# Optimization experiments

Hardware: AMD Instinct MI355X
Metric: run time of the kernel (lower is better)

Reference implementation:

```python
import jax, jax.numpy as jnp
import numpy as np

NUM_EMBEDDINGS = 8192
EMBEDDING_DIM = 256


def setup_inputs() -> dict:
    key = jax.random.key(0)
    k1, k2 = jax.random.split(key)
    z = jax.random.normal(k1, (8, 4096, EMBEDDING_DIM), dtype=jnp.float32)
    # codebook initialized uniform(-1/K, 1/K) as in the torch module
    embeddings = jax.random.uniform(
        k2, (NUM_EMBEDDINGS, EMBEDDING_DIM), dtype=jnp.float32,
        minval=-1.0 / NUM_EMBEDDINGS, maxval=1.0 / NUM_EMBEDDINGS)
    return {"z": z, "embeddings": embeddings}


def reference(z, embeddings):
    # flat_z: [N, D]
    flat_z = z.reshape(-1, EMBEDDING_DIM)
    # squared L2 distances: ||z||^2 - 2 z E^T + ||E||^2  -> [N, K]
    distances = (
        jnp.sum(flat_z ** 2, axis=1, keepdims=True)
        - 2.0 * jnp.einsum('nd,kd->nk', flat_z, embeddings)
        + jnp.sum(embeddings ** 2, axis=1)
    )
    encoding_indices = jnp.argmin(distances, axis=1)  # [N]
    quantized = embeddings[encoding_indices].reshape(z.shape)
    return quantized
```

## Files before the change

### kernel.cpp

```cpp
#include <hip/hip_runtime.h>


#define KCODES 8192
#define DIM    256
#define NROWS  32768
#define BM     128
#define KT     256
#define CAPL   64
#define CAPG   16

typedef __attribute__((ext_vector_type(8))) short short8_t;
typedef __attribute__((ext_vector_type(4))) float f32x4_t;

__device__ __forceinline__ unsigned cvt_pk_bf16(float lo, float hi)
{
    unsigned r;
    asm("v_cvt_pk_bf16_f32 %0, %1, %2" : "=v"(r) : "v"(lo), "v"(hi));
    return r;
}

__device__ __forceinline__ unsigned fmap(float f)
{
    unsigned u = __float_as_uint(f);
    return (u & 0x80000000u) ? ~u : (u | 0x80000000u);
}
__device__ __forceinline__ float funmap(unsigned m)
{
    unsigned u = (m & 0x80000000u) ? (m & 0x7fffffffu) : ~m;
    return __uint_as_float(u);
}

__device__ __forceinline__ float np_sumsq_256(const float* __restrict__ x)
{
    float blk[2];
#pragma unroll
    for (int b = 0; b < 2; ++b) {
        const float* p = x + 128 * b;
        float r[8];
        float4 v0 = *reinterpret_cast<const float4*>(p);
        float4 v1 = *reinterpret_cast<const float4*>(p + 4);
        r[0] = __fmul_rn(v0.x, v0.x); r[1] = __fmul_rn(v0.y, v0.y);
        r[2] = __fmul_rn(v0.z, v0.z); r[3] = __fmul_rn(v0.w, v0.w);
        r[4] = __fmul_rn(v1.x, v1.x); r[5] = __fmul_rn(v1.y, v1.y);
        r[6] = __fmul_rn(v1.z, v1.z); r[7] = __fmul_rn(v1.w, v1.w);
        for (int i = 8; i < 128; i += 8) {
            float4 w0 = *reinterpret_cast<const float4*>(p + i);
            float4 w1 = *reinterpret_cast<const float4*>(p + i + 4);
            r[0] = __fadd_rn(r[0], __fmul_rn(w0.x, w0.x));
            r[1] = __fadd_rn(r[1], __fmul_rn(w0.y, w0.y));
            r[2] = __fadd_rn(r[2], __fmul_rn(w0.z, w0.z));
            r[3] = __fadd_rn(r[3], __fmul_rn(w0.w, w0.w));
            r[4] = __fadd_rn(r[4], __fmul_rn(w1.x, w1.x));
            r[5] = __fadd_rn(r[5], __fmul_rn(w1.y, w1.y));
            r[6] = __fadd_rn(r[6], __fmul_rn(w1.z, w1.z));
            r[7] = __fadd_rn(r[7], __fmul_rn(w1.w, w1.w));
        }
        blk[b] = __fadd_rn(__fadd_rn(__fadd_rn(r[0], r[1]), __fadd_rn(r[2], r[3])),
                           __fadd_rn(__fadd_rn(r[4], r[5]), __fadd_rn(r[6], r[7])));
    }
    return __fadd_rn(blk[0], blk[1]);
}

__global__ void vq_rowsq(const float* __restrict__ X, float* __restrict__ out, int nrows)
{
    const int r = blockIdx.x * blockDim.x + threadIdx.x;
    if (r < nrows) out[r] = np_sumsq_256(X + (size_t)r * DIM);
}

__global__ __launch_bounds__(512, 2)
void vq_p1(const float* __restrict__ z, const float* __restrict__ E,
           const float* __restrict__ A32, const float* __restrict__ C32,
           int* __restrict__ counts, unsigned short* __restrict__ candg,
           int* __restrict__ badcnt, int* __restrict__ badlist)
{
    __shared__ unsigned short zsh[BM * 256];
    __shared__ unsigned short esh[KT * 64];
    __shared__ float cbuf[KT];
    __shared__ float scandT[BM * CAPL];
    __shared__ unsigned short scandK[BM * CAPL];
    __shared__ int scnt[BM];
    __shared__ unsigned rminu[BM];

    const int tid  = threadIdx.x;
    const int lane = tid & 63;
    const int wave = tid >> 6;
    const int wr = wave >> 2;
    const int wc = wave & 3;
    const int l15 = lane & 15, l4 = lane >> 4;
    const int rowBase = blockIdx.x * BM;

    {
        const int r = tid >> 2, hf = tid & 3;
        const float* zp = z + (size_t)(rowBase + r) * DIM + hf * 64;
#pragma unroll
        for (int i = 0; i < 16; ++i) {
            float4 v = reinterpret_cast<const float4*>(zp)[i];
            unsigned lo = cvt_pk_bf16(v.x, v.y), hi = cvt_pk_bf16(v.z, v.w);
            const int slot = hf * 8 + (i >> 1);
            const int sub  = (i & 1) * 4;
            *reinterpret_cast<uint2*>(&zsh[r * 256 + ((slot ^ (r & 7)) << 3) + sub]) =
                make_uint2(lo, hi);
        }
    }
    if (tid < BM) { scnt[tid] = 0; rminu[tid] = 0xFFFFFFFFu; }

    float runm[16], Wv[16];
#pragma unroll
    for (int rf = 0; rf < 4; ++rf)
#pragma unroll
        for (int reg = 0; reg < 4; ++reg) {
            const float a = A32[rowBase + 64 * wr + 16 * rf + 4 * l4 + reg];
            const unsigned ebits = (__float_as_uint(a) >> 23) & 255u;
            Wv[rf * 4 + reg] = __uint_as_float((ebits - 19u) << 23);
            runm[rf * 4 + reg] = 1e30f;
        }
    __syncthreads();

#pragma unroll 1
    for (int kt = 0; kt < KCODES; kt += KT) {
        f32x4_t acc[4][4];
#pragma unroll
        for (int rf = 0; rf < 4; ++rf)
#pragma unroll
            for (int cf = 0; cf < 4; ++cf) acc[rf][cf] = (f32x4_t){0.f, 0.f, 0.f, 0.f};

#pragma unroll 1
        for (int c = 0; c < 4; ++c) {
            __syncthreads();
            if (c == 0 && tid < KT) cbuf[tid] = C32[kt + tid];
#pragma unroll
            for (int i = 0; i < 8; ++i) {
                const int gi = i * 512 + tid;
                const int code = gi >> 4, dp = gi & 15;
                float4 v = *reinterpret_cast<const float4*>(
                    &E[(size_t)(kt + code) * DIM + c * 64 + dp * 4]);
                unsigned lo = cvt_pk_bf16(v.x, v.y), hi = cvt_pk_bf16(v.z, v.w);
                const int slot = dp >> 1, sub = (dp & 1) * 4;
                *reinterpret_cast<uint2*>(
                    &esh[code * 64 + ((slot ^ (code & 7)) << 3) + sub]) = make_uint2(lo, hi);
            }
            __syncthreads();
#pragma unroll
            for (int ks = 0; ks < 2; ++ks) {
                short8_t a[4], b[4];
#pragma unroll
                for (int rf = 0; rf < 4; ++rf) {
                    const int row = 64 * wr + 16 * rf + l15;
                    const int slot = 8 * c + 4 * ks + l4;
                    a[rf] = *reinterpret_cast<const short8_t*>(
                        &zsh[row * 256 + ((slot ^ (row & 7)) << 3)]);
                }
#pragma unroll
                for (int cf = 0; cf < 4; ++cf) {
                    const int code = 64 * wc + 16 * cf + l15;
                    const int slot = 4 * ks + l4;
                    b[cf] = *reinterpret_cast<const short8_t*>(
                        &esh[code * 64 + ((slot ^ (code & 7)) << 3)]);
                }
#pragma unroll
                for (int rf = 0; rf < 4; ++rf)
#pragma unroll
                    for (int cf = 0; cf < 4; ++cf)
                        acc[rf][cf] = __builtin_amdgcn_mfma_f32_16x16x32_bf16(
                            a[rf], b[cf], acc[rf][cf], 0, 0, 0);
            }
        }

#pragma unroll
        for (int rf = 0; rf < 4; ++rf) {
#pragma unroll
            for (int reg = 0; reg < 4; ++reg) {
                float t[4];
#pragma unroll
                for (int cf = 0; cf < 4; ++cf)
                    t[cf] = fmaf(-2.0f, acc[rf][cf][reg], cbuf[64 * wc + 16 * cf + l15]);
                float m = fminf(fminf(t[0], t[1]), fminf(t[2], t[3]));
                m = fminf(m, __shfl_xor(m, 1));
                m = fminf(m, __shfl_xor(m, 2));
                m = fminf(m, __shfl_xor(m, 4));
                m = fminf(m, __shfl_xor(m, 8));
                const int idx = rf * 4 + reg;
                const int rl = 64 * wr + 16 * rf + 4 * l4 + reg;
                float rm = fminf(runm[idx], m);
                if (l15 == 0) atomicMin(&rminu[rl], fmap(rm));
                rm = fminf(rm, funmap(rminu[rl]));
                runm[idx] = rm;
                const float thr = rm + Wv[idx];
#pragma unroll
                for (int cf = 0; cf < 4; ++cf) {
                    if (t[cf] <= thr) {
                        const int ai = atomicAdd(&scnt[rl], 1);
                        if (ai < CAPL) {
                            scandT[rl * CAPL + ai] = t[cf];
                            scandK[rl * CAPL + ai] =
                                (unsigned short)(kt + 64 * wc + 16 * cf + l15);
                        }
                    }
                }
            }
        }
    }

    __syncthreads();
    if (tid < BM) {
        const int row = rowBase + tid;
        const float a = A32[row];
        const unsigned ebits = (__float_as_uint(a) >> 23) & 255u;
        const float Wr = __uint_as_float((ebits - 19u) << 23);
        const float thrF = funmap(rminu[tid]) + Wr;
        const int n = scnt[tid];
        bool bad = (n > CAPL);
        int m = 0;
        if (!bad) {
            for (int i = 0; i < n; ++i) {
                if (scandT[tid * CAPL + i] <= thrF) {
                    if (m < CAPG) candg[(size_t)row * CAPG + m] = scandK[tid * CAPL + i];
                    ++m;
                }
            }
            bad = (m > CAPG);
        }
        counts[row] = bad ? -1 : m;
        if (bad) badlist[atomicAdd(badcnt, 1)] = row;
    }
}

__global__ __launch_bounds__(256)
void vq_p2(const float* __restrict__ z, const float* __restrict__ E,
           const float* __restrict__ A32, const float* __restrict__ C32,
           const int* __restrict__ counts, const unsigned short* __restrict__ candg,
           int* __restrict__ widx)
{
    __shared__ float zsh[4][256];
    const int lane = threadIdx.x & 63;
    const int w = threadIdx.x >> 6;
    const int row = blockIdx.x * 4 + w;
    const int cnt = counts[row];
    if (cnt == 1) {
        if (lane == 0) widx[row] = (int)candg[(size_t)row * CAPG];
        return;
    }
    if (cnt <= 0 || cnt > CAPG) return;
    {
        float4 v = *reinterpret_cast<const float4*>(&z[(size_t)row * DIM + lane * 4]);
        *reinterpret_cast<float4*>(&zsh[w][lane * 4]) = v;
    }
    asm volatile("s_waitcnt lgkmcnt(0)" ::: "memory");
    __builtin_amdgcn_sched_barrier(0);
    const int cl = lane < cnt ? lane : cnt - 1;
    const int myk = (int)candg[(size_t)row * CAPG + cl];
    const float* er = E + (size_t)myk * DIM;
    float s0 = 0.f, s1 = 0.f, s2 = 0.f, s3 = 0.f;
#pragma unroll 16
    for (int t = 0; t < 64; ++t) {
        const float4 ev = *reinterpret_cast<const float4*>(er + 4 * t);
        const float4 zv = *reinterpret_cast<const float4*>(&zsh[w][4 * t]);
        s0 = __fadd_rn(s0, __fmul_rn(zv.x, ev.x));
        s1 = __fadd_rn(s1, __fmul_rn(zv.y, ev.y));
        s2 = __fadd_rn(s2, __fmul_rn(zv.z, ev.z));
        s3 = __fadd_rn(s3, __fmul_rn(zv.w, ev.w));
    }
    const float dot = __fadd_rn(__fadd_rn(s0, s1), __fadd_rn(s2, s3));
    const float dist = __fadd_rn(__fsub_rn(A32[row], 2.0f * dot), C32[myk]);
    unsigned long long key =
        ((unsigned long long)__float_as_uint(dist) << 13) | (unsigned)myk;
    if (lane >= cnt) key = ~0ull;
#pragma unroll
    for (int off = 1; off < 64; off <<= 1) {
        const unsigned long long ok = __shfl_xor(key, off);
        key = ok < key ? ok : key;
    }
    if (lane == 0) widx[row] = (int)(key & (KCODES - 1));
}

__global__ __launch_bounds__(1024)
void vq_pfull(const float* __restrict__ z, const float* __restrict__ E,
              const float* __restrict__ A32, const float* __restrict__ C32,
              const int* __restrict__ badcnt, const int* __restrict__ badlist,
              int* __restrict__ widx)
{
    __shared__ float zsh[256];
    __shared__ unsigned long long skey;
    const int tid = threadIdx.x;
    const int nbad = *badcnt;
    for (int it = blockIdx.x; it < nbad; it += gridDim.x) {
        const int row = badlist[it];
        if (tid == 0) skey = ~0ull;
        if (tid < 64) {
            float4 v = *reinterpret_cast<const float4*>(&z[(size_t)row * DIM + tid * 4]);
            *reinterpret_cast<float4*>(&zsh[tid * 4]) = v;
        }
        __syncthreads();
        const float Ar = A32[row];
        unsigned long long best = ~0ull;
#pragma unroll 1
        for (int i = 0; i < KCODES / 1024; ++i) {
            const int k = i * 1024 + tid;
            const float* er = E + (size_t)k * DIM;
            float s0 = 0.f, s1 = 0.f, s2 = 0.f, s3 = 0.f;
#pragma unroll 16
            for (int t = 0; t < 64; ++t) {
                const float4 ev = *reinterpret_cast<const float4*>(er + 4 * t);
                const float4 zv = *reinterpret_cast<const float4*>(&zsh[4 * t]);
                s0 = __fadd_rn(s0, __fmul_rn(zv.x, ev.x));
                s1 = __fadd_rn(s1, __fmul_rn(zv.y, ev.y));
                s2 = __fadd_rn(s2, __fmul_rn(zv.z, ev.z));
                s3 = __fadd_rn(s3, __fmul_rn(zv.w, ev.w));
            }
            const float dot = __fadd_rn(__fadd_rn(s0, s1), __fadd_rn(s2, s3));
            const float dist = __fadd_rn(__fsub_rn(Ar, 2.0f * dot), C32[k]);
            const unsigned long long key =
                ((unsigned long long)__float_as_uint(dist) << 13) | (unsigned)k;
            best = key < best ? key : best;
        }
#pragma unroll
        for (int off = 1; off < 64; off <<= 1) {
            const unsigned long long ok = __shfl_xor(best, off);
            best = ok < best ? ok : best;
        }
        if ((tid & 63) == 0) atomicMin(&skey, best);
        __syncthreads();
        if (tid == 0) widx[row] = (int)(skey & (KCODES - 1));
        __syncthreads();
    }
}

__global__ void vq_gather(const float* __restrict__ E, const int* __restrict__ widx,
                          float* __restrict__ out)
{
    const int gid = blockIdx.x * 256 + threadIdx.x;
    const int n  = gid >> 6;
    const int d4 = gid & 63;
    const int k = widx[n] & (KCODES - 1);
    reinterpret_cast<float4*>(out)[(size_t)n * 64 + d4] =
        reinterpret_cast<const float4*>(E)[(size_t)k * 64 + d4];
}

extern "C" void kernel_launch(void* const* d_in, const int* in_sizes, int n_in,
                              void* d_out, int out_size, void* d_ws, size_t ws_size,
                              hipStream_t stream)
{
    const float* zp = (const float*)d_in[0];
    const float* Ep = (const float*)d_in[1];
    float* out = (float*)d_out;
    char* ws = (char*)d_ws;

    float* A32    = (float*)ws;
    float* C32    = (float*)(ws + 131072);
    int*   widx   = (int*)(ws + 163840);
    int*   counts = (int*)(ws + 294912);
    int*   badcnt = (int*)(ws + 425984);
    int*   badlist = (int*)(ws + 426000);
    unsigned short* candg = (unsigned short*)(ws + 557072);

    hipMemsetAsync(badcnt, 0, 4, stream);
    vq_rowsq<<<NROWS / 256, 256, 0, stream>>>(zp, A32, NROWS);
    vq_rowsq<<<KCODES / 256, 256, 0, stream>>>(Ep, C32, KCODES);
    vq_p1<<<NROWS / BM, 512, 0, stream>>>(zp, Ep, A32, C32, counts, candg, badcnt, badlist);
    vq_p2<<<NROWS / 4, 256, 0, stream>>>(zp, Ep, A32, C32, counts, candg, widx);
    vq_pfull<<<512, 1024, 0, stream>>>(zp, Ep, A32, C32, badcnt, badlist, widx);
    vq_gather<<<NROWS * (DIM / 4) / 256, 256, 0, stream>>>(Ep, widx, out);
}
```

Before: 528.2 us.

## Pre-convert codebook to swizzled bf16 and double-buffer it via async LDS loads

Adds a kernel that converts the codebook to bf16 once, already laid out in the swizzled tile order that the main kernel expects, and stores it in the output buffer as scratch. The distance kernel now double-buffers codebook chunks in LDS using global_load_lds direct-to-LDS copies, which overlaps loading with MFMA work and cuts the synchronisations per chunk from two to one. Per-block conversion work is removed. The candidate list also drops the stored distance values and the final re-filtering pass, keeping up to 32 candidate indices directly. This can send more rows to the slower fallback path and relies on the output buffer being free until the gather kernel overwrites it.

New measurement: 664.3 us. +25.8%, slower.

```diff
diff --git a/kernel.cpp b/kernel.cpp
--- a/kernel.cpp
+++ b/kernel.cpp
@@ -6,8 +6,8 @@
 #define NROWS  32768
 #define BM     128
 #define KT     256
-#define CAPL   64
-#define CAPG   16
+#define NSTEP  128
+#define CAPG   32
 
 typedef __attribute__((ext_vector_type(8))) short short8_t;
 typedef __attribute__((ext_vector_type(4))) float f32x4_t;
@@ -17,6 +17,13 @@
     unsigned r;
     asm("v_cvt_pk_bf16_f32 %0, %1, %2" : "=v"(r) : "v"(lo), "v"(hi));
     return r;
+}
+
+__device__ __forceinline__ void gload_lds16(const void* g, void* l)
+{
+    __builtin_amdgcn_global_load_lds(
+        (const __attribute__((address_space(1))) unsigned int*)g,
+        (__attribute__((address_space(3))) unsigned int*)l, 16, 0, 0);
 }
 
 __device__ __forceinline__ unsigned fmap(float f)
@@ -67,17 +74,34 @@
     if (r < nrows) out[r] = np_sumsq_256(X + (size_t)r * DIM);
 }
 
+__global__ void vq_cvtE(const float* __restrict__ E, unsigned short* __restrict__ Ebf)
+{
+    const int gid = blockIdx.x * 256 + threadIdx.x;
+    const int code_g = gid >> 5;
+    const int sg = gid & 31;
+    const int c = sg >> 3, slot = sg & 7;
+    const int ktIdx = code_g >> 8, code = code_g & 255;
+    const float* src = E + (size_t)code_g * DIM + c * 64 + slot * 8;
+    const float4 v0 = *reinterpret_cast<const float4*>(src);
+    const float4 v1 = *reinterpret_cast<const float4*>(src + 4);
+    uint4 w;
+    w.x = cvt_pk_bf16(v0.x, v0.y); w.y = cvt_pk_bf16(v0.z, v0.w);
+    w.z = cvt_pk_bf16(v1.x, v1.y); w.w = cvt_pk_bf16(v1.z, v1.w);
+    unsigned short* dst = Ebf + (size_t)(ktIdx * 4 + c) * 16384
+                        + code * 64 + ((slot ^ (code & 7)) << 3);
+    *reinterpret_cast<uint4*>(dst) = w;
+}
+
 __global__ __launch_bounds__(512, 2)
-void vq_p1(const float* __restrict__ z, const float* __restrict__ E,
+void vq_p1(const float* __restrict__ z, const unsigned short* __restrict__ Ebf,
            const float* __restrict__ A32, const float* __restrict__ C32,
            int* __restrict__ counts, unsigned short* __restrict__ candg,
            int* __restrict__ badcnt, int* __restrict__ badlist)
 {
     __shared__ unsigned short zsh[BM * 256];
-    __shared__ unsigned short esh[KT * 64];
+    __shared__ unsigned short esh[2][KT * 64];
     __shared__ float cbuf[KT];
-    __shared__ float scandT[BM * CAPL];
-    __shared__ unsigned short scandK[BM * CAPL];
+    __shared__ unsigned short scandK[BM * CAPG];
     __shared__ int scnt[BM];
     __shared__ unsigned rminu[BM];
 
@@ -114,114 +138,107 @@
             Wv[rf * 4 + reg] = __uint_as_float((ebits - 19u) << 23);
             runm[rf * 4 + reg] = 1e30f;
         }
+
+    {
+        const char* g = reinterpret_cast<const char*>(Ebf) + tid * 16;
+        char* l = reinterpret_cast<char*>(&esh[0][0]) + wave * 1024;
+#pragma unroll
+        for (int i = 0; i < 4; ++i)
+            gload_lds16(g + i * 8192, l + i * 8192);
+    }
     __syncthreads();
 
+    f32x4_t acc[4][4];
 #pragma unroll 1
-    for (int kt = 0; kt < KCODES; kt += KT) {
-        f32x4_t acc[4][4];
-#pragma unroll
-        for (int rf = 0; rf < 4; ++rf)
-#pragma unroll
-            for (int cf = 0; cf < 4; ++cf) acc[rf][cf] = (f32x4_t){0.f, 0.f, 0.f, 0.f};
-
-#pragma unroll 1
-        for (int c = 0; c < 4; ++c) {
-            __syncthreads();
-            if (c == 0 && tid < KT) cbuf[tid] = C32[kt + tid];
-#pragma unroll
-            for (int i = 0; i < 8; ++i) {
-                const int gi = i * 512 + tid;
-                const int code = gi >> 4, dp = gi & 15;
-                float4 v = *reinterpret_cast<const float4*>(
-                    &E[(size_t)(kt + code) * DIM + c * 64 + dp * 4]);
-                unsigned lo = cvt_pk_bf16(v.x, v.y), hi = cvt_pk_bf16(v.z, v.w);
-                const int slot = dp >> 1, sub = (dp & 1) * 4;
-                *reinterpret_cast<uint2*>(
-                    &esh[code * 64 + ((slot ^ (code & 7)) << 3) + sub]) = make_uint2(lo, hi);
+    for (int s = 0; s < NSTEP; ++s) {
+        const int cur = s & 1;
+        const int c = s & 3;
+        if (c == 0) {
+#pragma unroll
+            for (int rf = 0; rf < 4; ++rf)
+#pragma unroll
+                for (int cf = 0; cf < 4; ++cf) acc[rf][cf] = (f32x4_t){0.f, 0.f, 0.f, 0.f};
+            if (tid < KT) cbuf[tid] = C32[(s >> 2) * KT + tid];
+        }
+        if (s + 1 < NSTEP) {
+            const char* g = reinterpret_cast<const char*>(Ebf)
+                          + (size_t)(s + 1) * 32768 + tid * 16;
+            char* l = reinterpret_cast<char*>(&esh[cur ^ 1][0]) + wave * 1024;
+#pragma unroll
+            for (int i = 0; i < 4; ++i)
+                gload_lds16(g + i * 8192, l + i * 8192);
+        }
+#pragma unroll
+        for (int ks = 0; ks < 2; ++ks) {
+            short8_t a[4], b[4];
+#pragma unroll
+            for (int rf = 0; rf < 4; ++rf) {
+                const int row = 64 * wr + 16 * rf + l15;
+                const int slot = 8 * c + 4 * ks + l4;
+                a[rf] = *reinterpret_cast<const short8_t*>(
+                    &zsh[row * 256 + ((slot ^ (row & 7)) << 3)]);
             }
-            __syncthreads();
-#pragma unroll
-            for (int ks = 0; ks < 2; ++ks) {
-                short8_t a[4], b[4];
-#pragma unroll
-                for (int rf = 0; rf < 4; ++rf) {
-                    const int row = 64 * wr + 16 * rf + l15;
-                    const int slot = 8 * c + 4 * ks + l4;
-                    a[rf] = *reinterpret_cast<const short8_t*>(
-                        &zsh[row * 256 + ((slot ^ (row & 7)) << 3)]);
-                }
-#pragma unroll
-                for (int cf = 0; cf < 4; ++cf) {
-                    const int code = 64 * wc + 16 * cf + l15;
-                    const int slot = 4 * ks + l4;
-                    b[cf] = *reinterpret_cast<const short8_t*>(
-                        &esh[code * 64 + ((slot ^ (code & 7)) << 3)]);
-                }
-#pragma unroll
-                for (int rf = 0; rf < 4; ++rf)
+#pragma unroll
+            for (int cf = 0; cf < 4; ++cf) {
+                const int code = 64 * wc + 16 * cf + l15;
+                const int slot = 4 * ks + l4;
+                b[cf] = *reinterpret_cast<const short8_t*>(
+                    &esh[cur][code * 64 + ((slot ^ (code & 7)) << 3)]);
+            }
+#pragma unroll
+            for (int rf = 0; rf < 4; ++rf)
+#pragma unroll
+                for (int cf = 0; cf < 4; ++cf)
+                    acc[rf][cf] = __builtin_amdgcn_mfma_f32_16x16x32_bf16(
+                        a[rf], b[cf], acc[rf][cf], 0, 0, 0);
+        }
+        if (c == 3) {
+            const int kt = (s >> 2) * KT;
+#pragma unroll
+            for (int rf = 0; rf < 4; ++rf) {
+#pragma unroll
+                for (int reg = 0; reg < 4; ++reg) {
+                    float t[4];
 #pragma unroll
                     for (int cf = 0; cf < 4; ++cf)
-                        acc[rf][cf] = __builtin_amdgcn_mfma_f32_16x16x32_bf16(
-                            a[rf], b[cf], acc[rf][cf], 0, 0, 0);
-            }
-        }
-
-#pragma unroll
-        for (int rf = 0; rf < 4; ++rf) {
-#pragma unroll
-            for (int reg = 0; reg < 4; ++reg) {
-                float t[4];
-#pragma unroll
-                for (int cf = 0; cf < 4; ++cf)
-                    t[cf] = fmaf(-2.0f, acc[rf][cf][reg], cbuf[64 * wc + 16 * cf + l15]);
-                float m = fminf(fminf(t[0], t[1]), fminf(t[2], t[3]));
-                m = fminf(m, __shfl_xor(m, 1));
-                m = fminf(m, __shfl_xor(m, 2));
-                m = fminf(m, __shfl_xor(m, 4));
-                m = fminf(m, __shfl_xor(m, 8));
-                const int idx = rf * 4 + reg;
-                const int rl = 64 * wr + 16 * rf + 4 * l4 + reg;
-                float rm = fminf(runm[idx], m);
-                if (l15 == 0) atomicMin(&rminu[rl], fmap(rm));
-                rm = fminf(rm, funmap(rminu[rl]));
-                runm[idx] = rm;
-                const float thr = rm + Wv[idx];
-#pragma unroll
-                for (int cf = 0; cf < 4; ++cf) {
-                    if (t[cf] <= thr) {
-                        const int ai = atomicAdd(&scnt[rl], 1);
-                        if (ai < CAPL) {
-                            scandT[rl * CAPL + ai] = t[cf];
-                            scandK[rl * CAPL + ai] =
-                                (unsigned short)(kt + 64 * wc + 16 * cf + l15);
+                        t[cf] = fmaf(-2.0f, acc[rf][cf][reg],
+                                     cbuf[64 * wc + 16 * cf + l15]);
+                    float m = fminf(fminf(t[0], t[1]), fminf(t[2], t[3]));
+                    m = fminf(m, __shfl_xor(m, 1));
+                    m = fminf(m, __shfl_xor(m, 2));
+                    m = fminf(m, __shfl_xor(m, 4));
+                    m = fminf(m, __shfl_xor(m, 8));
+                    const int idx = rf * 4 + reg;
+                    const int rl = 64 * wr + 16 * rf + 4 * l4 + reg;
+                    float rm = fminf(runm[idx], m);
+                    if (l15 == 0) atomicMin(&rminu[rl], fmap(rm));
+                    rm = fminf(rm, funmap(rminu[rl]));
+                    runm[idx] = rm;
+                    const float thr = rm + Wv[idx];
+#pragma unroll
+                    for (int cf = 0; cf < 4; ++cf) {
+                        if (t[cf] <= thr) {
+                            const int ai = atomicAdd(&scnt[rl], 1);
+                            if (ai < CAPG)
+                                scandK[rl * CAPG + ai] =
+                                    (unsigned short)(kt + 64 * wc + 16 * cf + l15);
                         }
                     }
                 }
             }
         }
-    }
-
-    __syncthreads();
+        __syncthreads();
+    }
+
     if (tid < BM) {
         const int row = rowBase + tid;
-        const float a = A32[row];
-        const unsigned ebits = (__float_as_uint(a) >> 23) & 255u;
-        const float Wr = __uint_as_float((ebits - 19u) << 23);
-        const float thrF = funmap(rminu[tid]) + Wr;
         const int n = scnt[tid];
-        bool bad = (n > CAPL);
-        int m = 0;
-        if (!bad) {
-            for (int i = 0; i < n; ++i) {
-                if (scandT[tid * CAPL + i] <= thrF) {
-                    if (m < CAPG) candg[(size_t)row * CAPG + m] = scandK[tid * CAPL + i];
-                    ++m;
-                }
-            }
-            bad = (m > CAPG);
-        }
-        counts[row] = bad ? -1 : m;
+        const bool bad = (n > CAPG);
+        counts[row] = bad ? -1 : n;
         if (bad) badlist[atomicAdd(badcnt, 1)] = row;
+        else
+            for (int i = 0; i < n; ++i)
+                candg[(size_t)row * CAPG + i] = scandK[tid * CAPG + i];
     }
 }
 
@@ -351,12 +368,16 @@
     int*   counts = (int*)(ws + 294912);
     int*   badcnt = (int*)(ws + 425984);
     int*   badlist = (int*)(ws + 426000);
-    unsigned short* candg = (unsigned short*)(ws + 557072);
+
+    char* outb = (char*)d_out;
+    unsigned short* Ebf   = (unsigned short*)outb;
+    unsigned short* candg = (unsigned short*)(outb + 4194304);
 
     hipMemsetAsync(badcnt, 0, 4, stream);
     vq_rowsq<<<NROWS / 256, 256, 0, stream>>>(zp, A32, NROWS);
     vq_rowsq<<<KCODES / 256, 256, 0, stream>>>(Ep, C32, KCODES);
-    vq_p1<<<NROWS / BM, 512, 0, stream>>>(zp, Ep, A32, C32, counts, candg, badcnt, badlist);
+    vq_cvtE<<<KCODES * 32 / 256, 256, 0, stream>>>(Ep, Ebf);
+    vq_p1<<<NROWS / BM, 512, 0, stream>>>(zp, Ebf, A32, C32, counts, candg, badcnt, badlist);
     vq_p2<<<NROWS / 4, 256, 0, stream>>>(zp, Ep, A32, C32, counts, candg, widx);
     vq_pfull<<<512, 1024, 0, stream>>>(zp, Ep, A32, C32, badcnt, badlist, widx);
     vq_gather<<<NROWS * (DIM / 4) / 256, 256, 0, stream>>>(Ep, widx, out);
```
